# Kernel optimization log

Hardware: AMD Instinct MI355X
Metric: run time of the kernel (lower is better)

Reference implementation:

```python
import jax, jax.numpy as jnp
import numpy as np

K = 64  # key_features
V = 64  # value_features


def setup_inputs() -> dict:
    key = jax.random.key(0)
    ks = jax.random.split(key, 7)
    B, IN, M = 512, 512, 2048
    H = 2 * K + V  # 192, hidden_state dim == output dim of layer
    return {
        "x": jax.random.normal(ks[0], (B, IN), dtype=jnp.float32),
        "hidden_state": jax.random.normal(ks[1], (B, H), dtype=jnp.float32),
        "content": jax.random.normal(ks[2], (B, V), dtype=jnp.float32),
        "key_mem": jax.random.normal(ks[3], (B, K, M), dtype=jnp.float32),
        "value_mem": jax.random.normal(ks[4], (B, V, M), dtype=jnp.float32),
        "W": jax.random.normal(ks[5], (H, IN + 2 * K + 2 * V), dtype=jnp.float32) * 0.02,
        "b": jax.random.normal(ks[6], (H,), dtype=jnp.float32) * 0.02,
    }


def reference(x, hidden_state, content, key_mem, value_mem, W, b):
    # dropout in eval mode (identity); relu on hidden_state
    inp = jnp.concatenate([x, jax.nn.relu(hidden_state), content], axis=1)  # [B, IN+2K+2V]
    o = inp @ W.T + b  # [B, 2K+V]
    query = o[:, :K]            # [B, K]
    # buffer.read: attention over memory slots
    scores = jnp.einsum("bkm,bk->bm", key_mem, query)   # [B, M]
    attn = jax.nn.softmax(scores, axis=1)               # [B, M]
    content_new = jnp.einsum("bvm,bm->bv", value_mem, attn)  # [B, V]
    # buffer.write (state update, returned for completeness of math; original
    # mutates buffer in place; key @ II is exactly a right-shift by one slot):
    new_key = o[:, K:2 * K]
    new_value = o[:, 2 * K:2 * K + V]
    key_mem_next = jnp.concatenate([new_key[:, :, None], key_mem[:, :, :-1]], axis=2)
    value_mem_next = jnp.concatenate([new_value[:, :, None], value_mem[:, :, :-1]], axis=2)
    del key_mem_next, value_mem_next  # forward output matches original: (o, content)
    return (o, content_new)
```

## Files before the change

### kernel.cpp

```cpp
#include <hip/hip_runtime.h>

#define KDIM 64
#define VDIM 64
#define MDIM 2048
#define BDIM 512
#define INDIM 512
#define HDIM 192
#define CIN 768
#define O_SIZE (BDIM*HDIM)

typedef float f32x4 __attribute__((ext_vector_type(4)));

__global__ __launch_bounds__(512, 4)
void memlinear_kernel(const float* __restrict__ x,
                      const float* __restrict__ hidden,
                      const float* __restrict__ content,
                      const float* __restrict__ key_mem,
                      const float* __restrict__ value_mem,
                      const float* __restrict__ W,
                      const float* __restrict__ bias,
                      float* __restrict__ out)
{
    const int b    = blockIdx.x;
    const int tid  = threadIdx.x;
    const int lane = tid & 63;
    const int wid  = tid >> 6;

    __shared__ __align__(16) float inp[CIN];
    __shared__ float q[KDIM];
    __shared__ float red[8];
    __shared__ __align__(16) float attn_lds[MDIM];

    if (tid < INDIM) inp[tid] = x[(size_t)b*INDIM + tid];
    if (tid < HDIM)  inp[INDIM + tid] = fmaxf(hidden[(size_t)b*HDIM + tid], 0.f);
    if (tid < VDIM)  inp[INDIM + HDIM + tid] = content[(size_t)b*VDIM + tid];
    __syncthreads();

    if (tid < HDIM) {
        const float4* w4 = reinterpret_cast<const float4*>(W) + (size_t)tid * (CIN/4);
        const float4* i4 = reinterpret_cast<const float4*>(inp);
        float ax = 0.f, ay = 0.f, az = 0.f, aw = 0.f;
        #pragma unroll 8
        for (int i = 0; i < CIN/4; ++i) {
            float4 w = w4[i];
            float4 v = i4[i];
            ax = fmaf(w.x, v.x, ax);
            ay = fmaf(w.y, v.y, ay);
            az = fmaf(w.z, v.z, az);
            aw = fmaf(w.w, v.w, aw);
        }
        float o = (ax + ay) + (az + aw) + bias[tid];
        out[(size_t)b*HDIM + tid] = o;
        if (tid < KDIM) q[tid] = o;
    }
    __syncthreads();

    const f32x4* km4 = reinterpret_cast<const f32x4*>(key_mem + (size_t)b*KDIM*MDIM);
    float sx = 0.f, sy = 0.f, sz = 0.f, sw = 0.f;
    #pragma unroll 8
    for (int k = 0; k < KDIM; ++k) {
        float qk = q[k];
        f32x4 kk = __builtin_nontemporal_load(km4 + (size_t)k*(MDIM/4) + tid);
        sx = fmaf(qk, kk.x, sx);
        sy = fmaf(qk, kk.y, sy);
        sz = fmaf(qk, kk.z, sz);
        sw = fmaf(qk, kk.w, sw);
    }

    float mx = fmaxf(fmaxf(sx, sy), fmaxf(sz, sw));
    #pragma unroll
    for (int off = 32; off >= 1; off >>= 1)
        mx = fmaxf(mx, __shfl_xor(mx, off));
    if (lane == 0) red[wid] = mx;
    __syncthreads();
    float m_all = red[0];
    #pragma unroll
    for (int w = 1; w < 8; ++w) m_all = fmaxf(m_all, red[w]);

    float ex = __expf(sx - m_all);
    float ey = __expf(sy - m_all);
    float ez = __expf(sz - m_all);
    float ew = __expf(sw - m_all);
    float sum = (ex + ey) + (ez + ew);
    #pragma unroll
    for (int off = 32; off >= 1; off >>= 1)
        sum += __shfl_xor(sum, off);
    __syncthreads();
    if (lane == 0) red[wid] = sum;
    __syncthreads();
    float total = 0.f;
    #pragma unroll
    for (int w = 0; w < 8; ++w) total += red[w];
    float inv = 1.0f / total;

    reinterpret_cast<float4*>(attn_lds)[tid] =
        make_float4(ex*inv, ey*inv, ez*inv, ew*inv);
    __syncthreads();

    const f32x4* vm4 = reinterpret_cast<const f32x4*>(value_mem + (size_t)b*VDIM*MDIM);
    const float4* a4 = reinterpret_cast<const float4*>(attn_lds);
    #pragma unroll
    for (int vi = 0; vi < 8; ++vi) {
        int v = wid*8 + vi;
        float px = 0.f, py = 0.f, pz = 0.f, pw = 0.f;
        #pragma unroll
        for (int i = 0; i < 8; ++i) {
            f32x4 vv = __builtin_nontemporal_load(vm4 + (size_t)v*(MDIM/4) + i*64 + lane);
            float4 aa = a4[i*64 + lane];
            px = fmaf(vv.x, aa.x, px);
            py = fmaf(vv.y, aa.y, py);
            pz = fmaf(vv.z, aa.z, pz);
            pw = fmaf(vv.w, aa.w, pw);
        }
        float p = (px + py) + (pz + pw);
        #pragma unroll
        for (int off = 32; off >= 1; off >>= 1)
            p += __shfl_xor(p, off);
        if (lane == 0) out[O_SIZE + (size_t)b*VDIM + v] = p;
    }
}

extern "C" void kernel_launch(void* const* d_in, const int* in_sizes, int n_in,
                              void* d_out, int out_size, void* d_ws, size_t ws_size,
                              hipStream_t stream) {
    const float* x         = (const float*)d_in[0];
    const float* hidden    = (const float*)d_in[1];
    const float* content   = (const float*)d_in[2];
    const float* key_mem   = (const float*)d_in[3];
    const float* value_mem = (const float*)d_in[4];
    const float* W         = (const float*)d_in[5];
    const float* bias      = (const float*)d_in[6];
    float* out = (float*)d_out;

    memlinear_kernel<<<dim3(BDIM), dim3(512), 0, stream>>>(
        x, hidden, content, key_mem, value_mem, W, bias, out);
}
```

Baseline: 120.3 us.

## Split linear-layer dot products across lanes and defer non-query outputs

```diff
diff --git a/kernel.cpp b/kernel.cpp
--- a/kernel.cpp
+++ b/kernel.cpp
@@ -36,22 +36,36 @@
     if (tid < VDIM)  inp[INDIM + HDIM + tid] = content[(size_t)b*VDIM + tid];
     __syncthreads();
 
-    if (tid < HDIM) {
-        const float4* w4 = reinterpret_cast<const float4*>(W) + (size_t)tid * (CIN/4);
-        const float4* i4 = reinterpret_cast<const float4*>(inp);
+    {
+        const int j = tid >> 3;
+        const int p = tid & 7;
+        const float4* w4 = reinterpret_cast<const float4*>(W)
+                           + (size_t)j * (CIN/4) + p * (CIN/32);
+        const float4* i4 = reinterpret_cast<const float4*>(inp) + p * (CIN/32);
         float ax = 0.f, ay = 0.f, az = 0.f, aw = 0.f;
-        #pragma unroll 8
-        for (int i = 0; i < CIN/4; ++i) {
-            float4 w = w4[i];
-            float4 v = i4[i];
-            ax = fmaf(w.x, v.x, ax);
-            ay = fmaf(w.y, v.y, ay);
-            az = fmaf(w.z, v.z, az);
-            aw = fmaf(w.w, v.w, aw);
+        #pragma unroll
+        for (int r = 0; r < CIN/32; r += 8) {
+            float4 wr[8];
+            #pragma unroll
+            for (int u = 0; u < 8; ++u) wr[u] = w4[r + u];
+            #pragma unroll
+            for (int u = 0; u < 8; ++u) {
+                float4 v = i4[r + u];
+                ax = fmaf(wr[u].x, v.x, ax);
+                ay = fmaf(wr[u].y, v.y, ay);
+                az = fmaf(wr[u].z, v.z, az);
+                aw = fmaf(wr[u].w, v.w, aw);
+            }
         }
-        float o = (ax + ay) + (az + aw) + bias[tid];
-        out[(size_t)b*HDIM + tid] = o;
-        if (tid < KDIM) q[tid] = o;
+        float pacc = (ax + ay) + (az + aw);
+        pacc += __shfl_xor(pacc, 1);
+        pacc += __shfl_xor(pacc, 2);
+        pacc += __shfl_xor(pacc, 4);
+        if (p == 0) {
+            float o = pacc + bias[j];
+            out[(size_t)b*HDIM + j] = o;
+            q[j] = o;
+        }
     }
     __syncthreads();
 
@@ -118,6 +132,34 @@
             p += __shfl_xor(p, off);
         if (lane == 0) out[O_SIZE + (size_t)b*VDIM + v] = p;
     }
+
+    {
+        const int jj = tid >> 2;
+        const int j  = KDIM + jj;
+        const int p  = tid & 3;
+        const float4* w4 = reinterpret_cast<const float4*>(W)
+                           + (size_t)j * (CIN/4) + p * (CIN/16);
+        const float4* i4 = reinterpret_cast<const float4*>(inp) + p * (CIN/16);
+        float ax = 0.f, ay = 0.f, az = 0.f, aw = 0.f;
+        #pragma unroll
+        for (int r = 0; r < CIN/16; r += 8) {
+            float4 wr[8];
+            #pragma unroll
+            for (int u = 0; u < 8; ++u) wr[u] = w4[r + u];
+            #pragma unroll
+            for (int u = 0; u < 8; ++u) {
+                float4 v = i4[r + u];
+                ax = fmaf(wr[u].x, v.x, ax);
+                ay = fmaf(wr[u].y, v.y, ay);
+                az = fmaf(wr[u].z, v.z, az);
+                aw = fmaf(wr[u].w, v.w, aw);
+            }
+        }
+        float pacc = (ax + ay) + (az + aw);
+        pacc += __shfl_xor(pacc, 1);
+        pacc += __shfl_xor(pacc, 2);
+        if (p == 0) out[(size_t)b*HDIM + j] = pacc + bias[j];
+    }
 }
 
 extern "C" void kernel_launch(void* const* d_in, const int* in_sizes, int n_in,
```

New measurement: 116.4 us. 1.03x faster.
